# Kernel optimization log

Hardware: AMD Instinct MI355X
Metric: run time of the kernel (lower is better)

Reference implementation:

```python
import jax, jax.numpy as jnp
import numpy as np


def _gcn_conv(h, src, dst, W, b, n):
    # PyG GCNConv: x @ W, then symmetric-normalized aggregation with self-loops
    deg = jax.ops.segment_sum(jnp.ones(src.shape[0], h.dtype), dst, num_segments=n)
    dinv = jax.lax.rsqrt(jnp.maximum(deg, 1.0))  # deg >= 1 because self-loops are included
    norm = dinv[src] * dinv[dst]                 # [E]
    m = (h @ W)[src] * norm[:, None]             # gather + scale
    return jax.ops.segment_sum(m, dst, num_segments=n) + b


def setup_inputs() -> dict:
    key = jax.random.key(0)
    N, E, F, H, L, V = 50000, 800000, 128, 256, 64, 128
    ks = jax.random.split(key, 16)
    s = lambda fan_in: 1.0 / np.sqrt(fan_in)
    return {
        "x": jax.random.randint(ks[0], (N,), 0, V),
        "edge_index": jax.random.randint(ks[1], (2, E), 0, N),
        "eps": jax.random.normal(ks[2], (N, L), jnp.float32),
        "emb": jax.random.normal(ks[3], (V, F), jnp.float32),
        "W1": jax.random.normal(ks[4], (F, H), jnp.float32) * s(F),
        "b1": jnp.zeros((H,), jnp.float32),
        "W2": jax.random.normal(ks[5], (H, H), jnp.float32) * s(H),
        "b2": jnp.zeros((H,), jnp.float32),
        "Wmu": jax.random.normal(ks[6], (H, L), jnp.float32) * s(H),
        "bmu": jnp.zeros((L,), jnp.float32),
        "Wlv": jax.random.normal(ks[7], (H, L), jnp.float32) * s(H),
        "blv": jnp.zeros((L,), jnp.float32),
        "W3": jax.random.normal(ks[8], (L, H), jnp.float32) * s(L),
        "b3": jnp.zeros((H,), jnp.float32),
        "W4": jax.random.normal(ks[9], (H, V), jnp.float32) * s(H),
        "b4": jnp.zeros((V,), jnp.float32),
        "Wcap": jax.random.normal(ks[10], (L, 1), jnp.float32) * s(L),
        "bcap": jnp.zeros((1,), jnp.float32),
    }


def reference(x, edge_index, eps, emb, W1, b1, W2, b2, Wmu, bmu, Wlv, blv, W3, b3, W4, b4, Wcap, bcap):
    n = x.shape[0]
    loops = jnp.arange(n, dtype=edge_index.dtype)
    src = jnp.concatenate([edge_index[0], loops])  # add self-loops once, reuse
    dst = jnp.concatenate([edge_index[1], loops])

    h = emb[x]                                      # [N, F] embedding lookup
    h = jax.nn.relu(_gcn_conv(h, src, dst, W1, b1, n))
    h = jax.nn.relu(_gcn_conv(h, src, dst, W2, b2, n))
    mu = h @ Wmu + bmu
    logvar = h @ Wlv + blv
    z = mu + eps * jnp.exp(0.5 * logvar)            # reparameterize
    recon_x = jax.nn.relu(z @ W3 + b3) @ W4 + b4    # decode
    capitalize = jax.nn.sigmoid(z @ Wcap + bcap)
    return recon_x, capitalize, mu, logvar
```

## Files before the change

### kernel.cpp

```cpp
#include <hip/hip_runtime.h>
#include <math.h>


typedef __attribute__((ext_vector_type(8))) short bf16x8;
typedef __attribute__((ext_vector_type(8))) unsigned short u16x8;
typedef __attribute__((ext_vector_type(4))) float f32x4;

__device__ inline unsigned short f2bf(float x) {
    unsigned u = __float_as_uint(x);
    return (unsigned short)((u + 0x7FFFu + ((u >> 16) & 1u)) >> 16);
}
__device__ inline float bf2f(unsigned short h) {
    return __uint_as_float(((unsigned)h) << 16);
}

__global__ __launch_bounds__(256) void k_deg_count(const int* __restrict__ dst,
                                                   int* __restrict__ degint, int E) {
    int e = blockIdx.x * 256 + threadIdx.x;
    if (e < E) atomicAdd(&degint[dst[e]], 1);
}

#define SCAN_BLOCK 1024
__global__ __launch_bounds__(SCAN_BLOCK) void k_scan_local(
        const int* __restrict__ degint, int* __restrict__ row_ptr,
        int* __restrict__ bsum, float* __restrict__ dinv, int N) {
    __shared__ int s[SCAN_BLOCK];
    int gid = blockIdx.x * SCAN_BLOCK + threadIdx.x;
    int d = (gid < N) ? (degint[gid] + 1) : 0;
    if (gid < N) dinv[gid] = rsqrtf((float)d);
    s[threadIdx.x] = d;
    __syncthreads();
    for (int off = 1; off < SCAN_BLOCK; off <<= 1) {
        int t = (threadIdx.x >= off) ? s[threadIdx.x - off] : 0;
        __syncthreads();
        s[threadIdx.x] += t;
        __syncthreads();
    }
    if (gid < N) row_ptr[gid] = s[threadIdx.x] - d;
    if (threadIdx.x == SCAN_BLOCK - 1) bsum[blockIdx.x] = s[SCAN_BLOCK - 1];
}

__global__ __launch_bounds__(256) void k_scan_add(int* __restrict__ row_ptr,
                                                  const int* __restrict__ bsum,
                                                  int N, int T) {
    const int gid = blockIdx.x * 256 + threadIdx.x;
    const int myb = (blockIdx.x * 256) / SCAN_BLOCK;
    const int lane = threadIdx.x & 63;
    int v = (lane < myb) ? bsum[lane] : 0;
    v += __shfl_xor(v, 1, 64);
    v += __shfl_xor(v, 2, 64);
    v += __shfl_xor(v, 4, 64);
    v += __shfl_xor(v, 8, 64);
    v += __shfl_xor(v, 16, 64);
    v += __shfl_xor(v, 32, 64);
    if (gid < N) row_ptr[gid] += v;
    if (gid == 0) row_ptr[N] = T;
}

__global__ __launch_bounds__(256) void k_fill(
        const int* __restrict__ src, const int* __restrict__ dst,
        const int* __restrict__ x, const float* __restrict__ dinv,
        const int* __restrict__ row_ptr, int* __restrict__ cursor,
        int4* __restrict__ pack, int E, int N) {
    const int base = (blockIdx.x * 256 + threadIdx.x) * 4;
#pragma unroll
    for (int j = 0; j < 4; ++j) {
        int e = base + j;
        if (e < E) {
            int s = src[e], d = dst[e];
            float w = dinv[s] * dinv[d];
            int pos = row_ptr[d] + atomicAdd(&cursor[d], 1);
            pack[pos] = make_int4(__float_as_int(w), s, x[s], 0);
        } else if (e < E + N) {
            int i = e - E;
            float di = dinv[i];
            int pos = row_ptr[i] + atomicAdd(&cursor[i], 1);
            pack[pos] = make_int4(__float_as_int(di * di), i, x[i], 0);
        }
    }
}

__global__ __launch_bounds__(256) void k_cvt_all(
        const float* __restrict__ B0, unsigned short* __restrict__ h0, int K0, int N0,
        const float* __restrict__ B1, unsigned short* __restrict__ h1, int K1, int N1,
        const float* __restrict__ B2, unsigned short* __restrict__ h2, int K2, int N2,
        const float* __restrict__ B3, unsigned short* __restrict__ h3, int K3, int N3,
        const float* __restrict__ B4, unsigned short* __restrict__ h4, int K4, int N4) {
    const float* B; unsigned short* Bh; int K, Ncol;
    switch (blockIdx.y) {
        case 0: B = B0; Bh = h0; K = K0; Ncol = N0; break;
        case 1: B = B1; Bh = h1; K = K1; Ncol = N1; break;
        case 2: B = B2; Bh = h2; K = K2; Ncol = N2; break;
        case 3: B = B3; Bh = h3; K = K3; Ncol = N3; break;
        default: B = B4; Bh = h4; K = K4; Ncol = N4; break;
    }
    int i = blockIdx.x * 256 + threadIdx.x;
    if (i >= K * Ncol) return;
    int k = i / Ncol, n = i - k * Ncol;
    Bh[(long)n * K + k] = f2bf(B[i]);
}

__global__ __launch_bounds__(256) void k_gemm_f32t(
        const float* __restrict__ A, const float* __restrict__ B,
        unsigned short* __restrict__ CbT, int M, int K, int Ncol) {
    constexpr int BM = 64, BN = 64, BK = 16;
    __shared__ float As[BK][BM];
    __shared__ float Bs[BK][BN];
    const int tid = threadIdx.x;
    const int tx = tid & 15, ty = tid >> 4;
    const int rowBase = blockIdx.x * BM;
    const int colBase = blockIdx.y * BN;
    const int lr = tid >> 2, lc4 = tid & 3;
    const int br = tid >> 4, bc4 = tid & 15;
    const int arow = rowBase + lr;
    const int K4 = K >> 2, N4 = Ncol >> 2;
    const float4* A4 = (const float4*)A;
    const float4* B4 = (const float4*)B;
    float acc[4][4] = {{0.f}};
    for (int k0 = 0; k0 < K; k0 += BK) {
        float4 av = make_float4(0.f, 0.f, 0.f, 0.f);
        if (arow < M) av = A4[(long)arow * K4 + (k0 >> 2) + lc4];
        As[lc4 * 4 + 0][lr] = av.x;
        As[lc4 * 4 + 1][lr] = av.y;
        As[lc4 * 4 + 2][lr] = av.z;
        As[lc4 * 4 + 3][lr] = av.w;
        float4 bv = B4[(long)(k0 + br) * N4 + (colBase >> 2) + bc4];
        *(float4*)&Bs[br][bc4 * 4] = bv;
        __syncthreads();
#pragma unroll
        for (int k = 0; k < BK; ++k) {
            float4 a4v = *(const float4*)&As[k][ty * 4];
            float4 b4v = *(const float4*)&Bs[k][tx * 4];
            float aa[4] = {a4v.x, a4v.y, a4v.z, a4v.w};
            float bb[4] = {b4v.x, b4v.y, b4v.z, b4v.w};
#pragma unroll
            for (int i = 0; i < 4; ++i)
#pragma unroll
                for (int j = 0; j < 4; ++j)
                    acc[i][j] = fmaf(aa[i], bb[j], acc[i][j]);
        }
        __syncthreads();
    }
#pragma unroll
    for (int i = 0; i < 4; ++i) {
        int row = rowBase + ty * 4 + i;
        if (row < M) {
#pragma unroll
            for (int c = 0; c < 4; ++c) {
                int col = colBase + tx * 4 + c;
                CbT[(long)col * M + row] = f2bf(acc[i][c]);
            }
        }
    }
}

__global__ __launch_bounds__(256) void k_coef(
        const int4* __restrict__ pack, const int* __restrict__ row_ptr,
        unsigned short* __restrict__ cb, int N) {
    const int wave = threadIdx.x >> 6;
    const int lane = threadIdx.x & 63;
    const int node = blockIdx.x * 4 + wave;
    if (node >= N) return;
    const int tok0 = lane, tok1 = lane + 64;
    float c0 = 0.f, c1 = 0.f;
    const int beg = row_ptr[node], end = row_ptr[node + 1];
    int e = beg;
    for (; e + 4 <= end; e += 4) {
        int4 p0 = pack[e];
        int4 p1 = pack[e + 1];
        int4 p2 = pack[e + 2];
        int4 p3 = pack[e + 3];
        c0 += (p0.z == tok0) ? __int_as_float(p0.x) : 0.f;
        c1 += (p0.z == tok1) ? __int_as_float(p0.x) : 0.f;
        c0 += (p1.z == tok0) ? __int_as_float(p1.x) : 0.f;
        c1 += (p1.z == tok1) ? __int_as_float(p1.x) : 0.f;
        c0 += (p2.z == tok0) ? __int_as_float(p2.x) : 0.f;
        c1 += (p2.z == tok1) ? __int_as_float(p2.x) : 0.f;
        c0 += (p3.z == tok0) ? __int_as_float(p3.x) : 0.f;
        c1 += (p3.z == tok1) ? __int_as_float(p3.x) : 0.f;
    }
    for (; e < end; ++e) {
        int4 p = pack[e];
        c0 += (p.z == tok0) ? __int_as_float(p.x) : 0.f;
        c1 += (p.z == tok1) ? __int_as_float(p.x) : 0.f;
    }
    const long base = (long)node * 128;
    cb[base + lane]      = f2bf(c0);
    cb[base + lane + 64] = f2bf(c1);
}

template<bool RELU>
__global__ __launch_bounds__(256) void k_gemm_bn128(
        const unsigned short* __restrict__ A, const unsigned short* __restrict__ Bt,
        const float* __restrict__ bias, unsigned short* __restrict__ Cb,
        int M, int K, int Ncol) {
    __shared__ unsigned short Ash[64][40];
    __shared__ unsigned short Bsh[128][40];
    const int tid = threadIdx.x;
    const int lane = tid & 63, w = tid >> 6;
    const int fr = lane & 15, quad = lane >> 4;
    const int wm0 = w * 16;
    const int rowBase = blockIdx.x * 64;
    const int colBase = blockIdx.y * 128;

    const int arow = tid >> 2;
    const int aseg = (tid & 3) << 3;
    int agrow = rowBase + arow; if (agrow >= M) agrow = M - 1;
    const long abase = (long)agrow * K + aseg;
    const int brow = tid >> 1;
    const int bseg = (tid & 1) << 4;
    const long bbase = (long)(colBase + brow) * K + bseg;

    f32x4 acc[8];
#pragma unroll
    for (int j = 0; j < 8; ++j) acc[j] = (f32x4){0.f, 0.f, 0.f, 0.f};

    for (int k0 = 0; k0 < K; k0 += 32) {
        *(bf16x8*)&Ash[arow][aseg]     = *(const bf16x8*)&A[abase + k0];
        *(bf16x8*)&Bsh[brow][bseg]     = *(const bf16x8*)&Bt[bbase + k0];
        *(bf16x8*)&Bsh[brow][bseg + 8] = *(const bf16x8*)&Bt[bbase + k0 + 8];
        __syncthreads();
        bf16x8 af = *(const bf16x8*)&Ash[wm0 + fr][quad * 8];
#pragma unroll
        for (int j = 0; j < 8; ++j) {
            bf16x8 bhf = *(const bf16x8*)&Bsh[j * 16 + fr][quad * 8];
            acc[j] = __builtin_amdgcn_mfma_f32_16x16x32_bf16(af, bhf, acc[j], 0, 0, 0);
        }
        __syncthreads();
    }

#pragma unroll
    for (int j = 0; j < 8; ++j) {
        const int col = colBase + j * 16 + fr;
        const float bv = bias[col];
#pragma unroll
        for (int r = 0; r < 4; ++r) {
            const int row = rowBase + wm0 + quad * 4 + r;
            if (row < M) {
                float v = acc[j][r] + bv;
                if (RELU) v = fmaxf(v, 0.f);
                Cb[(long)row * Ncol + col] = f2bf(v);
            }
        }
    }
}

__global__ __launch_bounds__(256) void k_gemm_tail(
        const unsigned short* __restrict__ A, const unsigned short* __restrict__ Wml,
        const unsigned short* __restrict__ W3t, const unsigned short* __restrict__ W4t,
        const float* __restrict__ bmu, const float* __restrict__ blv,
        const float* __restrict__ eps, const float* __restrict__ Wcap,
        const float* __restrict__ bcap, const float* __restrict__ b3,
        const float* __restrict__ b4, float* __restrict__ mu,
        float* __restrict__ lv, float* __restrict__ recon,
        float* __restrict__ cap, int M) {
    constexpr int K = 256;
    __shared__ unsigned short Ash[64][40];
    __shared__ unsigned short Bsh[256][40];
    __shared__ unsigned short Zs[64][72];
    __shared__ unsigned short Ts[64][264];
    const int tid = threadIdx.x;
    const int lane = tid & 63, w = tid >> 6;
    const int fr = lane & 15, quad = lane >> 4;
    const int wm0 = w * 16;
    const int rowBase = blockIdx.x * 64;

    {
        const int zr = tid >> 2, zc = (tid & 3) * 18;
#pragma unroll
        for (int c = 0; c < 18; ++c) Zs[zr][zc + c] = 0;
    }

    const int arow = tid >> 2;
    const int aseg = (tid & 3) << 3;
    int agrow = rowBase + arow; if (agrow >= M) agrow = M - 1;
    const long abase = (long)agrow * K + aseg;
    const int brow = tid >> 1;
    const int bseg = (tid & 1) << 4;
    const long bbase = (long)brow * K + bseg;

    f32x4 acc[8];
#pragma unroll
    for (int j = 0; j < 8; ++j) acc[j] = (f32x4){0.f, 0.f, 0.f, 0.f};

    for (int k0 = 0; k0 < K; k0 += 32) {
        *(bf16x8*)&Ash[arow][aseg]     = *(const bf16x8*)&A[abase + k0];
        *(bf16x8*)&Bsh[brow][bseg]     = *(const bf16x8*)&Wml[bbase + k0];
        *(bf16x8*)&Bsh[brow][bseg + 8] = *(const bf16x8*)&Wml[bbase + k0 + 8];
        __syncthreads();
        bf16x8 ahf = *(const bf16x8*)&Ash[wm0 + fr][quad * 8];
#pragma unroll
        for (int j = 0; j < 8; ++j) {
            bf16x8 bhf = *(const bf16x8*)&Bsh[j * 16 + fr][quad * 8];
            acc[j] = __builtin_amdgcn_mfma_f32_16x16x32_bf16(ahf, bhf, acc[j], 0, 0, 0);
        }
        __syncthreads();
    }

    float capacc[4] = {0.f, 0.f, 0.f, 0.f};
#pragma unroll
    for (int j = 0; j < 4; ++j) {
        const int c = j * 16 + fr;
        const float bm = bmu[c], bl = blv[c];
        const float wc = Wcap[c];
#pragma unroll
        for (int r = 0; r < 4; ++r) {
            const int rl = wm0 + quad * 4 + r;
            const int row = rowBase + rl;
            if (row < M) {
                const long o = (long)row * 64 + c;
                float mv = acc[j][r] + bm;
                float lvv = acc[j + 4][r] + bl;
                mu[o] = mv;
                lv[o] = lvv;
                float zz = fmaf(eps[o], expf(0.5f * lvv), mv);
                Zs[rl][c] = f2bf(zz);
                capacc[r] = fmaf(zz, wc, capacc[r]);
            }
        }
    }
    const float b0 = bcap[0];
#pragma unroll
    for (int r = 0; r < 4; ++r) {
        float v = capacc[r];
        v += __shfl_xor(v, 1, 64);
        v += __shfl_xor(v, 2, 64);
        v += __shfl_xor(v, 4, 64);
        v += __shfl_xor(v, 8, 64);
        if (fr == 0) {
            const int row = rowBase + wm0 + quad * 4 + r;
            if (row < M) cap[row] = 1.f / (1.f + expf(-(v + b0)));
        }
    }

    f32x4 acc1[16];
#pragma unroll
    for (int j = 0; j < 16; ++j) acc1[j] = (f32x4){0.f, 0.f, 0.f, 0.f};
    for (int k0 = 0; k0 < 64; k0 += 32) {
        {
            const long wb = (long)tid * 64 + k0;
            *(bf16x8*)&Bsh[tid][0]  = *(const bf16x8*)&W3t[wb];
            *(bf16x8*)&Bsh[tid][8]  = *(const bf16x8*)&W3t[wb + 8];
            *(bf16x8*)&Bsh[tid][16] = *(const bf16x8*)&W3t[wb + 16];
            *(bf16x8*)&Bsh[tid][24] = *(const bf16x8*)&W3t[wb + 24];
        }
        __syncthreads();
        bf16x8 af = *(const bf16x8*)&Zs[wm0 + fr][k0 + quad * 8];
#pragma unroll
        for (int j = 0; j < 16; ++j) {
            bf16x8 bf = *(const bf16x8*)&Bsh[j * 16 + fr][quad * 8];
            acc1[j] = __builtin_amdgcn_mfma_f32_16x16x32_bf16(af, bf, acc1[j], 0, 0, 0);
        }
        __syncthreads();
    }

#pragma unroll
    for (int j = 0; j < 16; ++j) {
        const int col = j * 16 + fr;
        const float bv = b3[col];
#pragma unroll
        for (int r = 0; r < 4; ++r) {
            const int rl = wm0 + quad * 4 + r;
            Ts[rl][col] = f2bf(fmaxf(acc1[j][r] + bv, 0.f));
        }
    }
    __syncthreads();

    f32x4 acc2[8];
#pragma unroll
    for (int j = 0; j < 8; ++j) acc2[j] = (f32x4){0.f, 0.f, 0.f, 0.f};
    const int br2 = tid >> 1;
    const int bs2 = (tid & 1) << 4;
    for (int k0 = 0; k0 < 256; k0 += 32) {
        const long wb = (long)br2 * 256 + k0 + bs2;
        *(bf16x8*)&Bsh[br2][bs2]     = *(const bf16x8*)&W4t[wb];
        *(bf16x8*)&Bsh[br2][bs2 + 8] = *(const bf16x8*)&W4t[wb + 8];
        __syncthreads();
        bf16x8 at = *(const bf16x8*)&Ts[wm0 + fr][k0 + quad * 8];
#pragma unroll
        for (int j = 0; j < 8; ++j) {
            bf16x8 bf = *(const bf16x8*)&Bsh[j * 16 + fr][quad * 8];
            acc2[j] = __builtin_amdgcn_mfma_f32_16x16x32_bf16(at, bf, acc2[j], 0, 0, 0);
        }
        __syncthreads();
    }

#pragma unroll
    for (int j = 0; j < 8; ++j) {
        const int col = j * 16 + fr;
        const float bv = b4[col];
#pragma unroll
        for (int r = 0; r < 4; ++r) {
            const int row = rowBase + wm0 + quad * 4 + r;
            if (row < M) recon[(long)row * 128 + col] = acc2[j][r] + bv;
        }
    }
}

__global__ __launch_bounds__(256) void k_agg_nb(
        const unsigned short* __restrict__ h1, const int* __restrict__ row_ptr,
        const int2* __restrict__ pk2, unsigned short* __restrict__ Ob, int N) {
    const int wave = threadIdx.x >> 6;
    const int lane = threadIdx.x & 63;
    const int node = blockIdx.x * 4 + wave;
    if (node >= N) return;
    const int half = lane >> 5;
    const int col  = lane & 31;
    const u16x8* hrow = (const u16x8*)h1;
    float acc[8] = {0.f, 0.f, 0.f, 0.f, 0.f, 0.f, 0.f, 0.f};
    const int beg = row_ptr[node], end = row_ptr[node + 1];
    int e = beg;
    for (; e + 8 <= end; e += 8) {
        int2 q0 = pk2[2 * (e + 0 + half)];
        int2 q1 = pk2[2 * (e + 2 + half)];
        int2 q2 = pk2[2 * (e + 4 + half)];
        int2 q3 = pk2[2 * (e + 6 + half)];
        u16x8 v0 = hrow[(long)q0.y * 32 + col];
        u16x8 v1 = hrow[(long)q1.y * 32 + col];
        u16x8 v2 = hrow[(long)q2.y * 32 + col];
        u16x8 v3 = hrow[(long)q3.y * 32 + col];
        float w0 = __int_as_float(q0.x), w1 = __int_as_float(q1.x);
        float w2 = __int_as_float(q2.x), w3 = __int_as_float(q3.x);
#pragma unroll
        for (int c = 0; c < 8; ++c) {
            acc[c] = fmaf(bf2f(v0[c]), w0, acc[c]);
            acc[c] = fmaf(bf2f(v1[c]), w1, acc[c]);
            acc[c] = fmaf(bf2f(v2[c]), w2, acc[c]);
            acc[c] = fmaf(bf2f(v3[c]), w3, acc[c]);
        }
    }
    for (; e + 2 <= end; e += 2) {
        int2 q = pk2[2 * (e + half)];
        float w = __int_as_float(q.x);
        u16x8 v = hrow[(long)q.y * 32 + col];
#pragma unroll
        for (int c = 0; c < 8; ++c) acc[c] = fmaf(bf2f(v[c]), w, acc[c]);
    }
    if (e < end) {
        int2 q = pk2[2 * e];
        float w = (half == 0) ? __int_as_float(q.x) : 0.f;
        u16x8 v = hrow[(long)q.y * 32 + col];
#pragma unroll
        for (int c = 0; c < 8; ++c) acc[c] = fmaf(bf2f(v[c]), w, acc[c]);
    }
#pragma unroll
    for (int c = 0; c < 8; ++c) acc[c] += __shfl_xor(acc[c], 32, 64);
    if (lane < 32) {
        u16x8 o;
#pragma unroll
        for (int c = 0; c < 8; ++c) o[c] = f2bf(acc[c]);
        ((u16x8*)Ob)[(long)node * 32 + col] = o;
    }
}

extern "C" void kernel_launch(void* const* d_in, const int* in_sizes, int n_in,
                              void* d_out, int out_size, void* d_ws, size_t ws_size,
                              hipStream_t stream) {
    const int*   x    = (const int*)d_in[0];
    const int*   ei   = (const int*)d_in[1];
    const float* eps  = (const float*)d_in[2];
    const float* emb  = (const float*)d_in[3];
    const float* W1   = (const float*)d_in[4];
    const float* b1   = (const float*)d_in[5];
    const float* W2   = (const float*)d_in[6];
    const float* b2   = (const float*)d_in[7];
    const float* Wmu  = (const float*)d_in[8];
    const float* bmu  = (const float*)d_in[9];
    const float* Wlv  = (const float*)d_in[10];
    const float* blv  = (const float*)d_in[11];
    const float* W3   = (const float*)d_in[12];
    const float* b3   = (const float*)d_in[13];
    const float* W4   = (const float*)d_in[14];
    const float* b4   = (const float*)d_in[15];
    const float* Wcap = (const float*)d_in[16];
    const float* bcap = (const float*)d_in[17];

    const int N = in_sizes[0];
    const int E = in_sizes[1] / 2;
    const int H = in_sizes[5];
    const int L = in_sizes[9];
    const int V = in_sizes[15];
    const int F = in_sizes[4] / H;
    const int T = E + N;

    const int* src = ei;
    const int* dst = ei + E;

    char* w = (char*)d_ws;
    unsigned short* h1b  = (unsigned short*)w; w += (size_t)N * H * 2;
    unsigned short* a2b  = (unsigned short*)w; w += (size_t)N * H * 2;
    unsigned short* h2b  = (unsigned short*)w; w += (size_t)N * H * 2;
    unsigned short* cb   = (unsigned short*)w; w += (size_t)N * V * 2;
    int*   degint = (int*)w;   w += (size_t)N * 4;
    int*   cursor = (int*)w;   w += (size_t)N * 4;
    int*   rowp   = (int*)w;   w += (size_t)(N + 1) * 4;
    float* dinv   = (float*)w; w += (size_t)N * 4;
    int*   bsum   = (int*)w;   w += 256 * 4;
    int4*  pack   = (int4*)w;  w += (size_t)T * 16;
    unsigned short* tabT = (unsigned short*)w; w += (size_t)H * V * 2;
    unsigned short* W2t  = (unsigned short*)w; w += (size_t)H * H * 2;
    unsigned short* Wml  = (unsigned short*)w; w += (size_t)H * 2 * L * 2;
    unsigned short* W3t  = (unsigned short*)w; w += (size_t)L * H * 2;
    unsigned short* W4t  = (unsigned short*)w; w += (size_t)H * V * 2;

    float* outp    = (float*)d_out;
    float* recon   = outp;
    float* cap     = outp + (size_t)N * V;
    float* mu      = outp + (size_t)N * V + N;
    float* logvar  = mu + (size_t)N * L;

    const int nN  = (N + 255) / 256;
    const int nE  = (E + 255) / 256;
    const int nT4 = (T + 1023) / 1024;
    const int nSc = (N + SCAN_BLOCK - 1) / SCAN_BLOCK;
    const int gM64  = (N + 63) / 64;

    hipMemsetAsync(degint, 0, (size_t)N * 8, stream);
    k_deg_count<<<nE, 256, 0, stream>>>(dst, degint, E);
    k_scan_local<<<nSc, SCAN_BLOCK, 0, stream>>>(degint, rowp, bsum, dinv, N);
    k_scan_add<<<nN, 256, 0, stream>>>(rowp, bsum, N, T);
    k_fill<<<nT4, 256, 0, stream>>>(src, dst, x, dinv, rowp, cursor, pack, E, N);

    k_cvt_all<<<dim3((H * H + 255) / 256, 5), 256, 0, stream>>>(
        W2, W2t, H, H,
        Wmu, Wml, H, L,
        Wlv, Wml + (size_t)L * H, H, L,
        W3, W3t, L, H,
        W4, W4t, H, V);

    k_gemm_f32t<<<dim3(V / 64, H / 64), 256, 0, stream>>>(emb, W1, tabT, V, F, H);
    k_coef<<<(N + 3) / 4, 256, 0, stream>>>(pack, rowp, cb, N);
    k_gemm_bn128<true><<<dim3(gM64, H / 128), 256, 0, stream>>>(
        cb, tabT, b1, h1b, N, V, H);

    k_agg_nb<<<(N + 3) / 4, 256, 0, stream>>>(h1b, rowp, (const int2*)pack, a2b, N);
    k_gemm_bn128<true><<<dim3(gM64, H / 128), 256, 0, stream>>>(
        a2b, W2t, b2, h2b, N, H, H);

    k_gemm_tail<<<gM64, 256, 0, stream>>>(
        h2b, Wml, W3t, W4t, bmu, blv, eps, Wcap, bcap, b3, b4,
        mu, logvar, recon, cap, N);
}
```

Before: 387.2 us.

## Fuse sparse aggregation into subsequent GEMMs, keeping aggregated rows in LDS

Merges the per-node token coefficient pass into the layer-1 GEMM, and the layer-2 neighbor aggregation into the W2 GEMM. Each block aggregates 64 rows into shared memory and then multiplies them by the full 256-column weight, so the intermediate cb and a2b buffers are never written to or read from global memory. It also aliases shared buffers in the tail kernel. The trade-off is fewer waves per node during the gather (one wave handles 16 nodes in sequence), larger LDS footprints and 16 accumulators, which may lower occupancy and latency hiding for the irregular gather.

```diff
diff --git a/kernel.cpp b/kernel.cpp
--- a/kernel.cpp
+++ b/kernel.cpp
@@ -3,7 +3,6 @@
 
 
 typedef __attribute__((ext_vector_type(8))) short bf16x8;
-typedef __attribute__((ext_vector_type(8))) unsigned short u16x8;
 typedef __attribute__((ext_vector_type(4))) float f32x4;
 
 __device__ inline unsigned short f2bf(float x) {
@@ -154,92 +153,182 @@
     }
 }
 
-__global__ __launch_bounds__(256) void k_coef(
+__global__ __launch_bounds__(256) void k_coef_gemm(
         const int4* __restrict__ pack, const int* __restrict__ row_ptr,
-        unsigned short* __restrict__ cb, int N) {
-    const int wave = threadIdx.x >> 6;
-    const int lane = threadIdx.x & 63;
-    const int node = blockIdx.x * 4 + wave;
-    if (node >= N) return;
-    const int tok0 = lane, tok1 = lane + 64;
-    float c0 = 0.f, c1 = 0.f;
-    const int beg = row_ptr[node], end = row_ptr[node + 1];
-    int e = beg;
-    for (; e + 4 <= end; e += 4) {
-        int4 p0 = pack[e];
-        int4 p1 = pack[e + 1];
-        int4 p2 = pack[e + 2];
-        int4 p3 = pack[e + 3];
-        c0 += (p0.z == tok0) ? __int_as_float(p0.x) : 0.f;
-        c1 += (p0.z == tok1) ? __int_as_float(p0.x) : 0.f;
-        c0 += (p1.z == tok0) ? __int_as_float(p1.x) : 0.f;
-        c1 += (p1.z == tok1) ? __int_as_float(p1.x) : 0.f;
-        c0 += (p2.z == tok0) ? __int_as_float(p2.x) : 0.f;
-        c1 += (p2.z == tok1) ? __int_as_float(p2.x) : 0.f;
-        c0 += (p3.z == tok0) ? __int_as_float(p3.x) : 0.f;
-        c1 += (p3.z == tok1) ? __int_as_float(p3.x) : 0.f;
-    }
-    for (; e < end; ++e) {
-        int4 p = pack[e];
-        c0 += (p.z == tok0) ? __int_as_float(p.x) : 0.f;
-        c1 += (p.z == tok1) ? __int_as_float(p.x) : 0.f;
-    }
-    const long base = (long)node * 128;
-    cb[base + lane]      = f2bf(c0);
-    cb[base + lane + 64] = f2bf(c1);
-}
-
-template<bool RELU>
-__global__ __launch_bounds__(256) void k_gemm_bn128(
-        const unsigned short* __restrict__ A, const unsigned short* __restrict__ Bt,
-        const float* __restrict__ bias, unsigned short* __restrict__ Cb,
-        int M, int K, int Ncol) {
-    __shared__ unsigned short Ash[64][40];
-    __shared__ unsigned short Bsh[128][40];
+        const unsigned short* __restrict__ tabT, const float* __restrict__ bias,
+        unsigned short* __restrict__ Cb, int M) {
+    __shared__ __align__(16) char smem[37888];
+    unsigned short (*Bsh)[40] = (unsigned short (*)[40])smem;
+    unsigned short (*As)[136] = (unsigned short (*)[136])(smem + 20480);
     const int tid = threadIdx.x;
     const int lane = tid & 63, w = tid >> 6;
     const int fr = lane & 15, quad = lane >> 4;
     const int wm0 = w * 16;
     const int rowBase = blockIdx.x * 64;
-    const int colBase = blockIdx.y * 128;
-
-    const int arow = tid >> 2;
-    const int aseg = (tid & 3) << 3;
-    int agrow = rowBase + arow; if (agrow >= M) agrow = M - 1;
-    const long abase = (long)agrow * K + aseg;
-    const int brow = tid >> 1;
-    const int bseg = (tid & 1) << 4;
-    const long bbase = (long)(colBase + brow) * K + bseg;
-
-    f32x4 acc[8];
-#pragma unroll
-    for (int j = 0; j < 8; ++j) acc[j] = (f32x4){0.f, 0.f, 0.f, 0.f};
-
-    for (int k0 = 0; k0 < K; k0 += 32) {
-        *(bf16x8*)&Ash[arow][aseg]     = *(const bf16x8*)&A[abase + k0];
-        *(bf16x8*)&Bsh[brow][bseg]     = *(const bf16x8*)&Bt[bbase + k0];
-        *(bf16x8*)&Bsh[brow][bseg + 8] = *(const bf16x8*)&Bt[bbase + k0 + 8];
-        __syncthreads();
-        bf16x8 af = *(const bf16x8*)&Ash[wm0 + fr][quad * 8];
-#pragma unroll
-        for (int j = 0; j < 8; ++j) {
-            bf16x8 bhf = *(const bf16x8*)&Bsh[j * 16 + fr][quad * 8];
-            acc[j] = __builtin_amdgcn_mfma_f32_16x16x32_bf16(af, bhf, acc[j], 0, 0, 0);
-        }
-        __syncthreads();
-    }
-
-#pragma unroll
-    for (int j = 0; j < 8; ++j) {
-        const int col = colBase + j * 16 + fr;
+    const int tok0 = lane, tok1 = lane + 64;
+
+    for (int i = 0; i < 16; ++i) {
+        const int node = rowBase + wm0 + i;
+        float c0 = 0.f, c1 = 0.f;
+        if (node < M) {
+            const int beg = row_ptr[node], end = row_ptr[node + 1];
+            int e = beg;
+            for (; e + 4 <= end; e += 4) {
+                int4 p0 = pack[e];
+                int4 p1 = pack[e + 1];
+                int4 p2 = pack[e + 2];
+                int4 p3 = pack[e + 3];
+                c0 += (p0.z == tok0) ? __int_as_float(p0.x) : 0.f;
+                c1 += (p0.z == tok1) ? __int_as_float(p0.x) : 0.f;
+                c0 += (p1.z == tok0) ? __int_as_float(p1.x) : 0.f;
+                c1 += (p1.z == tok1) ? __int_as_float(p1.x) : 0.f;
+                c0 += (p2.z == tok0) ? __int_as_float(p2.x) : 0.f;
+                c1 += (p2.z == tok1) ? __int_as_float(p2.x) : 0.f;
+                c0 += (p3.z == tok0) ? __int_as_float(p3.x) : 0.f;
+                c1 += (p3.z == tok1) ? __int_as_float(p3.x) : 0.f;
+            }
+            for (; e < end; ++e) {
+                int4 p = pack[e];
+                c0 += (p.z == tok0) ? __int_as_float(p.x) : 0.f;
+                c1 += (p.z == tok1) ? __int_as_float(p.x) : 0.f;
+            }
+        }
+        As[wm0 + i][lane]      = f2bf(c0);
+        As[wm0 + i][lane + 64] = f2bf(c1);
+    }
+    __syncthreads();
+
+    f32x4 acc[16];
+#pragma unroll
+    for (int j = 0; j < 16; ++j) acc[j] = (f32x4){0.f, 0.f, 0.f, 0.f};
+    for (int k0 = 0; k0 < 128; k0 += 32) {
+        const long wb = (long)tid * 128 + k0;
+        *(bf16x8*)&Bsh[tid][0]  = *(const bf16x8*)&tabT[wb];
+        *(bf16x8*)&Bsh[tid][8]  = *(const bf16x8*)&tabT[wb + 8];
+        *(bf16x8*)&Bsh[tid][16] = *(const bf16x8*)&tabT[wb + 16];
+        *(bf16x8*)&Bsh[tid][24] = *(const bf16x8*)&tabT[wb + 24];
+        __syncthreads();
+        bf16x8 af = *(const bf16x8*)&As[wm0 + fr][k0 + quad * 8];
+#pragma unroll
+        for (int j = 0; j < 16; ++j) {
+            bf16x8 bfv = *(const bf16x8*)&Bsh[j * 16 + fr][quad * 8];
+            acc[j] = __builtin_amdgcn_mfma_f32_16x16x32_bf16(af, bfv, acc[j], 0, 0, 0);
+        }
+        __syncthreads();
+    }
+
+#pragma unroll
+    for (int j = 0; j < 16; ++j) {
+        const int col = j * 16 + fr;
         const float bv = bias[col];
 #pragma unroll
         for (int r = 0; r < 4; ++r) {
             const int row = rowBase + wm0 + quad * 4 + r;
             if (row < M) {
-                float v = acc[j][r] + bv;
-                if (RELU) v = fmaxf(v, 0.f);
-                Cb[(long)row * Ncol + col] = f2bf(v);
+                float v = fmaxf(acc[j][r] + bv, 0.f);
+                Cb[(long)row * 256 + col] = f2bf(v);
+            }
+        }
+    }
+}
+
+__global__ __launch_bounds__(256) void k_agg_gemm(
+        const unsigned short* __restrict__ h1, const int* __restrict__ row_ptr,
+        const int2* __restrict__ pk2, const unsigned short* __restrict__ W2t,
+        const float* __restrict__ bias, unsigned short* __restrict__ Cb, int M) {
+    __shared__ __align__(16) char smem[54272];
+    unsigned short (*Bsh)[40]  = (unsigned short (*)[40])smem;
+    unsigned short (*As)[264]  = (unsigned short (*)[264])(smem + 20480);
+    const int tid = threadIdx.x;
+    const int lane = tid & 63, w = tid >> 6;
+    const int fr = lane & 15, quad = lane >> 4;
+    const int wm0 = w * 16;
+    const int rowBase = blockIdx.x * 64;
+    const ushort4* h4 = (const ushort4*)h1;
+
+    for (int i = 0; i < 16; ++i) {
+        const int node = rowBase + wm0 + i;
+        float ax = 0.f, ay = 0.f, az = 0.f, aw2 = 0.f;
+        if (node < M) {
+            const int beg = row_ptr[node], end = row_ptr[node + 1];
+            int e = beg;
+            for (; e + 8 <= end; e += 8) {
+                int2 q0 = pk2[2 * e],       q1 = pk2[2 * (e + 1)];
+                int2 q2 = pk2[2 * (e + 2)], q3 = pk2[2 * (e + 3)];
+                int2 q4 = pk2[2 * (e + 4)], q5 = pk2[2 * (e + 5)];
+                int2 q6 = pk2[2 * (e + 6)], q7 = pk2[2 * (e + 7)];
+                ushort4 v0 = h4[(long)q0.y * 64 + lane];
+                ushort4 v1 = h4[(long)q1.y * 64 + lane];
+                ushort4 v2 = h4[(long)q2.y * 64 + lane];
+                ushort4 v3 = h4[(long)q3.y * 64 + lane];
+                ushort4 v4 = h4[(long)q4.y * 64 + lane];
+                ushort4 v5 = h4[(long)q5.y * 64 + lane];
+                ushort4 v6 = h4[(long)q6.y * 64 + lane];
+                ushort4 v7 = h4[(long)q7.y * 64 + lane];
+                float w0 = __int_as_float(q0.x), w1 = __int_as_float(q1.x);
+                float w2 = __int_as_float(q2.x), w3 = __int_as_float(q3.x);
+                float w4 = __int_as_float(q4.x), w5 = __int_as_float(q5.x);
+                float w6 = __int_as_float(q6.x), w7 = __int_as_float(q7.x);
+                ax = fmaf(bf2f(v0.x), w0, ax); ay = fmaf(bf2f(v0.y), w0, ay);
+                az = fmaf(bf2f(v0.z), w0, az); aw2 = fmaf(bf2f(v0.w), w0, aw2);
+                ax = fmaf(bf2f(v1.x), w1, ax); ay = fmaf(bf2f(v1.y), w1, ay);
+                az = fmaf(bf2f(v1.z), w1, az); aw2 = fmaf(bf2f(v1.w), w1, aw2);
+                ax = fmaf(bf2f(v2.x), w2, ax); ay = fmaf(bf2f(v2.y), w2, ay);
+                az = fmaf(bf2f(v2.z), w2, az); aw2 = fmaf(bf2f(v2.w), w2, aw2);
+                ax = fmaf(bf2f(v3.x), w3, ax); ay = fmaf(bf2f(v3.y), w3, ay);
+                az = fmaf(bf2f(v3.z), w3, az); aw2 = fmaf(bf2f(v3.w), w3, aw2);
+                ax = fmaf(bf2f(v4.x), w4, ax); ay = fmaf(bf2f(v4.y), w4, ay);
+                az = fmaf(bf2f(v4.z), w4, az); aw2 = fmaf(bf2f(v4.w), w4, aw2);
+                ax = fmaf(bf2f(v5.x), w5, ax); ay = fmaf(bf2f(v5.y), w5, ay);
+                az = fmaf(bf2f(v5.z), w5, az); aw2 = fmaf(bf2f(v5.w), w5, aw2);
+                ax = fmaf(bf2f(v6.x), w6, ax); ay = fmaf(bf2f(v6.y), w6, ay);
+                az = fmaf(bf2f(v6.z), w6, az); aw2 = fmaf(bf2f(v6.w), w6, aw2);
+                ax = fmaf(bf2f(v7.x), w7, ax); ay = fmaf(bf2f(v7.y), w7, ay);
+                az = fmaf(bf2f(v7.z), w7, az); aw2 = fmaf(bf2f(v7.w), w7, aw2);
+            }
+            for (; e < end; ++e) {
+                int2 q = pk2[2 * e];
+                float w0 = __int_as_float(q.x);
+                ushort4 v = h4[(long)q.y * 64 + lane];
+                ax = fmaf(bf2f(v.x), w0, ax); ay = fmaf(bf2f(v.y), w0, ay);
+                az = fmaf(bf2f(v.z), w0, az); aw2 = fmaf(bf2f(v.w), w0, aw2);
+            }
+        }
+        ushort4 o;
+        o.x = f2bf(ax); o.y = f2bf(ay); o.z = f2bf(az); o.w = f2bf(aw2);
+        *(ushort4*)&As[wm0 + i][lane * 4] = o;
+    }
+    __syncthreads();
+
+    f32x4 acc[16];
+#pragma unroll
+    for (int j = 0; j < 16; ++j) acc[j] = (f32x4){0.f, 0.f, 0.f, 0.f};
+    for (int k0 = 0; k0 < 256; k0 += 32) {
+        const long wb = (long)tid * 256 + k0;
+        *(bf16x8*)&Bsh[tid][0]  = *(const bf16x8*)&W2t[wb];
+        *(bf16x8*)&Bsh[tid][8]  = *(const bf16x8*)&W2t[wb + 8];
+        *(bf16x8*)&Bsh[tid][16] = *(const bf16x8*)&W2t[wb + 16];
+        *(bf16x8*)&Bsh[tid][24] = *(const bf16x8*)&W2t[wb + 24];
+        __syncthreads();
+        bf16x8 af = *(const bf16x8*)&As[wm0 + fr][k0 + quad * 8];
+#pragma unroll
+        for (int j = 0; j < 16; ++j) {
+            bf16x8 bfv = *(const bf16x8*)&Bsh[j * 16 + fr][quad * 8];
+            acc[j] = __builtin_amdgcn_mfma_f32_16x16x32_bf16(af, bfv, acc[j], 0, 0, 0);
+        }
+        __syncthreads();
+    }
+
+#pragma unroll
+    for (int j = 0; j < 16; ++j) {
+        const int col = j * 16 + fr;
+        const float bv = bias[col];
+#pragma unroll
+        for (int r = 0; r < 4; ++r) {
+            const int row = rowBase + wm0 + quad * 4 + r;
+            if (row < M) {
+                float v = fmaxf(acc[j][r] + bv, 0.f);
+                Cb[(long)row * 256 + col] = f2bf(v);
             }
         }
     }
@@ -255,10 +344,11 @@
         float* __restrict__ lv, float* __restrict__ recon,
         float* __restrict__ cap, int M) {
     constexpr int K = 256;
-    __shared__ unsigned short Ash[64][40];
-    __shared__ unsigned short Bsh[256][40];
-    __shared__ unsigned short Zs[64][72];
-    __shared__ unsigned short Ts[64][264];
+    __shared__ __align__(16) char smem[54272];
+    unsigned short (*Bsh)[40] = (unsigned short (*)[40])smem;
+    unsigned short (*Ash)[40] = (unsigned short (*)[40])(smem + 20480);
+    unsigned short (*Zs)[72]  = (unsigned short (*)[72])(smem + 25600);
+    unsigned short (*Ts)[264] = (unsigned short (*)[264])(smem + 20480);
     const int tid = threadIdx.x;
     const int lane = tid & 63, w = tid >> 6;
     const int fr = lane & 15, quad = lane >> 4;
@@ -394,62 +484,6 @@
             const int row = rowBase + wm0 + quad * 4 + r;
             if (row < M) recon[(long)row * 128 + col] = acc2[j][r] + bv;
         }
-    }
-}
-
-__global__ __launch_bounds__(256) void k_agg_nb(
-        const unsigned short* __restrict__ h1, const int* __restrict__ row_ptr,
-        const int2* __restrict__ pk2, unsigned short* __restrict__ Ob, int N) {
-    const int wave = threadIdx.x >> 6;
-    const int lane = threadIdx.x & 63;
-    const int node = blockIdx.x * 4 + wave;
-    if (node >= N) return;
-    const int half = lane >> 5;
-    const int col  = lane & 31;
-    const u16x8* hrow = (const u16x8*)h1;
-    float acc[8] = {0.f, 0.f, 0.f, 0.f, 0.f, 0.f, 0.f, 0.f};
-    const int beg = row_ptr[node], end = row_ptr[node + 1];
-    int e = beg;
-    for (; e + 8 <= end; e += 8) {
-        int2 q0 = pk2[2 * (e + 0 + half)];
-        int2 q1 = pk2[2 * (e + 2 + half)];
-        int2 q2 = pk2[2 * (e + 4 + half)];
-        int2 q3 = pk2[2 * (e + 6 + half)];
-        u16x8 v0 = hrow[(long)q0.y * 32 + col];
-        u16x8 v1 = hrow[(long)q1.y * 32 + col];
-        u16x8 v2 = hrow[(long)q2.y * 32 + col];
-        u16x8 v3 = hrow[(long)q3.y * 32 + col];
-        float w0 = __int_as_float(q0.x), w1 = __int_as_float(q1.x);
-        float w2 = __int_as_float(q2.x), w3 = __int_as_float(q3.x);
-#pragma unroll
-        for (int c = 0; c < 8; ++c) {
-            acc[c] = fmaf(bf2f(v0[c]), w0, acc[c]);
-            acc[c] = fmaf(bf2f(v1[c]), w1, acc[c]);
-            acc[c] = fmaf(bf2f(v2[c]), w2, acc[c]);
-            acc[c] = fmaf(bf2f(v3[c]), w3, acc[c]);
-        }
-    }
-    for (; e + 2 <= end; e += 2) {
-        int2 q = pk2[2 * (e + half)];
-        float w = __int_as_float(q.x);
-        u16x8 v = hrow[(long)q.y * 32 + col];
-#pragma unroll
-        for (int c = 0; c < 8; ++c) acc[c] = fmaf(bf2f(v[c]), w, acc[c]);
-    }
-    if (e < end) {
-        int2 q = pk2[2 * e];
-        float w = (half == 0) ? __int_as_float(q.x) : 0.f;
-        u16x8 v = hrow[(long)q.y * 32 + col];
-#pragma unroll
-        for (int c = 0; c < 8; ++c) acc[c] = fmaf(bf2f(v[c]), w, acc[c]);
-    }
-#pragma unroll
-    for (int c = 0; c < 8; ++c) acc[c] += __shfl_xor(acc[c], 32, 64);
-    if (lane < 32) {
-        u16x8 o;
-#pragma unroll
-        for (int c = 0; c < 8; ++c) o[c] = f2bf(acc[c]);
-        ((u16x8*)Ob)[(long)node * 32 + col] = o;
     }
 }
 
@@ -488,9 +522,7 @@
 
     char* w = (char*)d_ws;
     unsigned short* h1b  = (unsigned short*)w; w += (size_t)N * H * 2;
-    unsigned short* a2b  = (unsigned short*)w; w += (size_t)N * H * 2;
     unsigned short* h2b  = (unsigned short*)w; w += (size_t)N * H * 2;
-    unsigned short* cb   = (unsigned short*)w; w += (size_t)N * V * 2;
     int*   degint = (int*)w;   w += (size_t)N * 4;
     int*   cursor = (int*)w;   w += (size_t)N * 4;
     int*   rowp   = (int*)w;   w += (size_t)(N + 1) * 4;
@@ -529,13 +561,10 @@
         W4, W4t, H, V);
 
     k_gemm_f32t<<<dim3(V / 64, H / 64), 256, 0, stream>>>(emb, W1, tabT, V, F, H);
-    k_coef<<<(N + 3) / 4, 256, 0, stream>>>(pack, rowp, cb, N);
-    k_gemm_bn128<true><<<dim3(gM64, H / 128), 256, 0, stream>>>(
-        cb, tabT, b1, h1b, N, V, H);
-
-    k_agg_nb<<<(N + 3) / 4, 256, 0, stream>>>(h1b, rowp, (const int2*)pack, a2b, N);
-    k_gemm_bn128<true><<<dim3(gM64, H / 128), 256, 0, stream>>>(
-        a2b, W2t, b2, h2b, N, H, H);
+    k_coef_gemm<<<gM64, 256, 0, stream>>>(pack, rowp, tabT, b1, h1b, N);
+
+    k_agg_gemm<<<gM64, 256, 0, stream>>>(
+        h1b, rowp, (const int2*)pack, W2t, b2, h2b, N);
 
     k_gemm_tail<<<gM64, 256, 0, stream>>>(
         h2b, Wml, W3t, W4t, bmu, blv, eps, Wcap, bcap, b3, b4,
```

Result: slower. 492.2 us (+27.1%).
